# Kernel tuning notes

Measured on AMD Instinct MI355X. Metric: run time of the kernel, lower is better.

Reference implementation:

```python
import jax, jax.numpy as jnp
import numpy as np

B, KPLUS1, D = 64, 513, 1024

def setup_inputs() -> dict:
    key = jax.random.key(0)
    k1, k2, k3 = jax.random.split(key, 3)
    x = jax.random.normal(k1, (B, KPLUS1, D), dtype=jnp.float32)
    # glorot-style scaled init for faithfulness in magnitude
    dense_weights = jax.random.normal(k2, (2 * D, D), dtype=jnp.float32) * (1.0 / np.sqrt(2 * D))
    dot_bias = jax.random.normal(k3, (D, 1), dtype=jnp.float32) * (1.0 / np.sqrt(D))
    return {"x": x, "dense_weights": dense_weights, "dot_bias": dot_bias}

def reference(x, dense_weights, dot_bias):
    # x: [B, K+1, D]; x[:,0] = sentence encoding u, x[:,1:] = knowledge z_t
    u = x[:, 0, :]            # [B, D]
    z = x[:, 1:, :]           # [B, K, D]
    d = z.shape[-1]
    # concat(z_t, u) @ W1 == z @ W1[:D] + u @ W1[D:], broadcast over K
    # (mathematically identical to the tile+concat+matmul in the original)
    w_z = dense_weights[:d, :]   # [D, D]
    w_u = dense_weights[d:, :]   # [D, D]
    m = jnp.tanh(jnp.einsum('bkd,de->bke', z, w_z)
                 + jnp.einsum('bd,de->be', u, w_u)[:, None, :])  # [B, K, D]
    q = jnp.einsum('bke,e->bk', m, dot_bias[:, 0])               # [B, K]
    return jax.nn.softmax(q, axis=-1)                            # [B, K]
```

## Files before the change

kernel.cpp:

```cpp
#include <hip/hip_runtime.h>
#include <hip/hip_bf16.h>


typedef __attribute__((ext_vector_type(8))) short short8;
typedef __attribute__((ext_vector_type(8))) _Float16 half8;
typedef __attribute__((ext_vector_type(4))) float f32x4;
typedef unsigned short ushort_t;

typedef const __attribute__((address_space(1))) void gvoid_t;
typedef __attribute__((address_space(3))) void lvoid_t;

__device__ __forceinline__ ushort_t f2bf(float f) {
    unsigned u = __float_as_uint(f);
    unsigned r = u + 0x7FFFu + ((u >> 16) & 1u);
    return (ushort_t)(r >> 16);
}
__device__ __forceinline__ float bf2f(ushort_t h) {
    return __uint_as_float(((unsigned)h) << 16);
}

__global__ __launch_bounds__(256) void k_prep_z16(const float* __restrict__ x,
                                                  _Float16* __restrict__ z_h) {
    const int idx8 = blockIdx.x * 256 + threadIdx.x;
    const int m = idx8 >> 7;
    const int c = (idx8 & 127) * 8;
    const int b = m >> 9, k = m & 511;
    const float* src = x + ((size_t)(b * 513 + 1 + k) << 10) + c;
    const float4 v0 = *(const float4*)src;
    const float4 v1 = *(const float4*)(src + 4);
    float vv[8] = {v0.x, v0.y, v0.z, v0.w, v1.x, v1.y, v1.z, v1.w};
    half8 hv;
#pragma unroll
    for (int i = 0; i < 8; ++i) hv[i] = (_Float16)vv[i];
    *(half8*)(z_h + (size_t)m * 1024 + c) = hv;
}

__global__ void k_prep_w16(const float* __restrict__ w,
                           _Float16* __restrict__ wzt) {
    __shared__ _Float16 th[64][66];
    const int k0 = blockIdx.x * 64;
    const int n0 = blockIdx.y * 64;
    const int t = threadIdx.x;
    const int lr = t >> 6;
    const int lc = t & 63;
#pragma unroll
    for (int r = 0; r < 16; ++r) {
        int kk = r * 4 + lr;
        th[kk][lc] = (_Float16)w[(size_t)(k0 + kk) * 1024 + n0 + lc];
    }
    __syncthreads();
#pragma unroll
    for (int r = 0; r < 16; ++r) {
        int nn = r * 4 + lr;
        wzt[(size_t)(n0 + nn) * 1024 + k0 + lc] = th[lc][nn];
    }
}

__global__ void k_hu(const float* __restrict__ x,
                     const float* __restrict__ w,
                     float* __restrict__ hu) {
    __shared__ float us[1024];
    const int b = blockIdx.y;
    const int e = blockIdx.x * 256 + threadIdx.x;
    for (int i = threadIdx.x; i < 1024; i += 256)
        us[i] = x[(size_t)b * 513 * 1024 + i];
    __syncthreads();
    const float* wu = w + (size_t)1024 * 1024;
    float acc = 0.f;
#pragma unroll 8
    for (int d = 0; d < 1024; ++d)
        acc = fmaf(us[d], wu[(size_t)d * 1024 + e], acc);
    hu[b * 1024 + e] = acc;
}

__global__ __launch_bounds__(256) void k_gemm6(
        const _Float16* __restrict__ z_h,
        const _Float16* __restrict__ wzt,
        const float* __restrict__ hu,
        const float* __restrict__ bias,
        float* __restrict__ qp) {
    __shared__ __align__(16) _Float16 As[128 * 64];
    __shared__ __align__(16) _Float16 Bs[128 * 64];
    __shared__ float qred[2][2][64];

    const int t = threadIdx.x;
    const int mtile = blockIdx.x;
    const int ntile = blockIdx.y;
    const int wid = t >> 6;
    const int l = t & 63;
    const int wm = wid >> 1;
    const int wn = wid & 1;
    const int lr = l & 15;
    const int g = l >> 4;

    const int rl = l >> 3;
    const int chunk = (l & 7) ^ rl;
    const int half = wid & 1;
    const _Float16* gsrc;
    _Float16* ldsT;
    if (wid < 2) {
        gsrc = z_h + (size_t)(mtile * 128 + half * 64 + rl) * 1024 + chunk * 8;
        ldsT = As + half * 4096;
    } else {
        gsrc = wzt + (size_t)(ntile * 128 + half * 64 + rl) * 1024 + chunk * 8;
        ldsT = Bs + half * 4096;
    }

    f32x4 acc[4][4] = {};

    for (int k0 = 0; k0 < 1024; k0 += 64) {
#pragma unroll
        for (int j = 0; j < 8; ++j) {
            __builtin_amdgcn_global_load_lds(
                (gvoid_t*)(gsrc + k0 + j * 8192),
                (lvoid_t*)((char*)ldsT + j * 1024),
                16, 0, 0);
        }
        __syncthreads();

#pragma unroll
        for (int ks = 0; ks < 2; ++ks) {
            half8 ah[4], bh[4];
            const int so = ((ks * 4 + g) ^ (lr & 7)) * 16;
#pragma unroll
            for (int i = 0; i < 4; ++i) {
                ah[i] = *(const half8*)((const char*)As + (wm * 64 + i * 16 + lr) * 128 + so);
                bh[i] = *(const half8*)((const char*)Bs + (wn * 64 + i * 16 + lr) * 128 + so);
            }
#pragma unroll
            for (int mi = 0; mi < 4; ++mi)
#pragma unroll
                for (int ni = 0; ni < 4; ++ni)
                    acc[mi][ni] = __builtin_amdgcn_mfma_f32_16x16x32_f16(
                        ah[mi], bh[ni], acc[mi][ni], 0, 0, 0);
        }
        __syncthreads();
    }

    const int lg = l >> 4;
    const int bbatch = mtile >> 2;
    float hu4[4], bias4[4];
#pragma unroll
    for (int ni = 0; ni < 4; ++ni) {
        int e = ntile * 128 + wn * 64 + ni * 16 + lr;
        hu4[ni] = hu[bbatch * 1024 + e];
        bias4[ni] = bias[e];
    }
#pragma unroll
    for (int mi = 0; mi < 4; ++mi) {
#pragma unroll
        for (int j = 0; j < 4; ++j) {
            float v = 0.f;
#pragma unroll
            for (int ni = 0; ni < 4; ++ni)
                v += tanhf(acc[mi][ni][j] + hu4[ni]) * bias4[ni];
            v += __shfl_xor(v, 1);
            v += __shfl_xor(v, 2);
            v += __shfl_xor(v, 4);
            v += __shfl_xor(v, 8);
            if (lr == 0)
                qred[wm][wn][mi * 16 + lg * 4 + j] = v;
        }
    }
    __syncthreads();
    if (t < 128) {
        const int wmr = t >> 6;
        const int rr = t & 63;
        float q = qred[wmr][0][rr] + qred[wmr][1][rr];
        qp[(size_t)ntile * 32768 + mtile * 128 + t] = q;
    }
}

__global__ void k_prep_w(const float* __restrict__ w,
                         ushort_t* __restrict__ wzt_hi,
                         ushort_t* __restrict__ wzt_lo) {
    __shared__ ushort_t th[64][66];
    __shared__ ushort_t tl[64][66];
    const int k0 = blockIdx.x * 64;
    const int n0 = blockIdx.y * 64;
    const int t = threadIdx.x;
    const int lr = t >> 6;
    const int lc = t & 63;
#pragma unroll
    for (int r = 0; r < 16; ++r) {
        int kk = r * 4 + lr;
        float f = w[(size_t)(k0 + kk) * 1024 + n0 + lc];
        ushort_t hi = f2bf(f);
        ushort_t lo = f2bf(f - bf2f(hi));
        th[kk][lc] = hi;
        tl[kk][lc] = lo;
    }
    __syncthreads();
#pragma unroll
    for (int r = 0; r < 16; ++r) {
        int nn = r * 4 + lr;
        wzt_hi[(size_t)(n0 + nn) * 1024 + k0 + lc] = th[lc][nn];
        wzt_lo[(size_t)(n0 + nn) * 1024 + k0 + lc] = tl[lc][nn];
    }
}

__global__ __launch_bounds__(256) void k_gemm(
        const float* __restrict__ x,
        const ushort_t* __restrict__ wzt_hi,
        const ushort_t* __restrict__ wzt_lo,
        const float* __restrict__ hu,
        const float* __restrict__ bias,
        float* __restrict__ qp) {
    __shared__ ushort_t As_hi[128][40];
    __shared__ ushort_t As_lo[128][40];
    __shared__ ushort_t Bs_hi[128][40];
    __shared__ ushort_t Bs_lo[128][40];
    __shared__ float qred[2][2][64];

    const int t = threadIdx.x;
    const int mtile = blockIdx.x;
    const int ntile = blockIdx.y;
    const int wid = t >> 6;
    const int l = t & 63;
    const int wm = wid >> 1;
    const int wn = wid & 1;

    f32x4 acc[4][4] = {};

    const int arow = t >> 3;
    const int acol = (t & 7) * 4;
    size_t abase[4];
#pragma unroll
    for (int it = 0; it < 4; ++it) {
        int m = mtile * 128 + arow + it * 32;
        int bb = m >> 9;
        int kk = m & 511;
        abase[it] = ((size_t)(bb * 513 + 1 + kk)) * 1024 + acol;
    }
    const int brow = t >> 2;
    const int bcol = (t & 3) * 8;
    const size_t bbase = (size_t)(ntile * 128 + brow) * 1024 + bcol;

    for (int k0 = 0; k0 < 1024; k0 += 32) {
#pragma unroll
        for (int it = 0; it < 4; ++it) {
            const float4 v = *(const float4*)(x + abase[it] + k0);
            ushort4 hv, lv;
            hv.x = f2bf(v.x); lv.x = f2bf(v.x - bf2f(hv.x));
            hv.y = f2bf(v.y); lv.y = f2bf(v.y - bf2f(hv.y));
            hv.z = f2bf(v.z); lv.z = f2bf(v.z - bf2f(hv.z));
            hv.w = f2bf(v.w); lv.w = f2bf(v.w - bf2f(hv.w));
            const int row = arow + it * 32;
            *(ushort4*)&As_hi[row][acol] = hv;
            *(ushort4*)&As_lo[row][acol] = lv;
        }
#pragma unroll
        for (int it = 0; it < 2; ++it) {
            const int row = brow + it * 64;
            const uint4 vh = *(const uint4*)(wzt_hi + bbase + (size_t)it * 64 * 1024 + k0);
            const uint4 vl = *(const uint4*)(wzt_lo + bbase + (size_t)it * 64 * 1024 + k0);
            *(uint4*)&Bs_hi[row][bcol] = vh;
            *(uint4*)&Bs_lo[row][bcol] = vl;
        }
        __syncthreads();

        const int lr = l & 15;
        const int lk = (l >> 4) * 8;
        short8 ah[4], al[4], bh[4], bl[4];
#pragma unroll
        for (int i = 0; i < 4; ++i) {
            ah[i] = *(const short8*)&As_hi[wm * 64 + i * 16 + lr][lk];
            al[i] = *(const short8*)&As_lo[wm * 64 + i * 16 + lr][lk];
            bh[i] = *(const short8*)&Bs_hi[wn * 64 + i * 16 + lr][lk];
            bl[i] = *(const short8*)&Bs_lo[wn * 64 + i * 16 + lr][lk];
        }
#pragma unroll
        for (int mi = 0; mi < 4; ++mi)
#pragma unroll
            for (int ni = 0; ni < 4; ++ni) {
                acc[mi][ni] = __builtin_amdgcn_mfma_f32_16x16x32_bf16(ah[mi], bh[ni], acc[mi][ni], 0, 0, 0);
                acc[mi][ni] = __builtin_amdgcn_mfma_f32_16x16x32_bf16(ah[mi], bl[ni], acc[mi][ni], 0, 0, 0);
                acc[mi][ni] = __builtin_amdgcn_mfma_f32_16x16x32_bf16(al[mi], bh[ni], acc[mi][ni], 0, 0, 0);
            }
        __syncthreads();
    }

    const int lr = l & 15;
    const int lg = l >> 4;
    const int bbatch = mtile >> 2;
    float hu4[4], bias4[4];
#pragma unroll
    for (int ni = 0; ni < 4; ++ni) {
        int e = ntile * 128 + wn * 64 + ni * 16 + lr;
        hu4[ni] = hu[bbatch * 1024 + e];
        bias4[ni] = bias[e];
    }
#pragma unroll
    for (int mi = 0; mi < 4; ++mi) {
#pragma unroll
        for (int j = 0; j < 4; ++j) {
            float v = 0.f;
#pragma unroll
            for (int ni = 0; ni < 4; ++ni)
                v += tanhf(acc[mi][ni][j] + hu4[ni]) * bias4[ni];
            v += __shfl_xor(v, 1);
            v += __shfl_xor(v, 2);
            v += __shfl_xor(v, 4);
            v += __shfl_xor(v, 8);
            if (lr == 0)
                qred[wm][wn][mi * 16 + lg * 4 + j] = v;
        }
    }
    __syncthreads();
    if (t < 128) {
        const int wmr = t >> 6;
        const int rr = t & 63;
        float q = qred[wmr][0][rr] + qred[wmr][1][rr];
        qp[(size_t)ntile * 32768 + mtile * 128 + t] = q;
    }
}

__global__ void k_softmax(const float* __restrict__ qp, float* __restrict__ out,
                          int nt) {
    const int b = blockIdx.x;
    const int k = threadIdx.x;
    float q = 0.f;
    for (int i = 0; i < nt; ++i)
        q += qp[(size_t)i * 32768 + b * 512 + k];

    __shared__ float redm[8];
    __shared__ float reds[8];
    const int wid = k >> 6;

    float m = q;
#pragma unroll
    for (int off = 32; off >= 1; off >>= 1)
        m = fmaxf(m, __shfl_xor(m, off));
    if ((k & 63) == 0) redm[wid] = m;
    __syncthreads();
    m = redm[0];
#pragma unroll
    for (int i = 1; i < 8; ++i) m = fmaxf(m, redm[i]);

    float p = expf(q - m);
    float s = p;
#pragma unroll
    for (int off = 32; off >= 1; off >>= 1)
        s += __shfl_xor(s, off);
    if ((k & 63) == 0) reds[wid] = s;
    __syncthreads();
    s = 0.f;
#pragma unroll
    for (int i = 0; i < 8; ++i) s += reds[i];

    out[b * 512 + k] = p / s;
}

extern "C" void kernel_launch(void* const* d_in, const int* in_sizes, int n_in,
                              void* d_out, int out_size, void* d_ws, size_t ws_size,
                              hipStream_t stream) {
    const float* x    = (const float*)d_in[0];
    const float* w    = (const float*)d_in[1];
    const float* bias = (const float*)d_in[2];
    float* out = (float*)d_out;

    char* ws = (char*)d_ws;
    const size_t ZN = (size_t)32768 * 1024;

    const size_t need = ZN * sizeof(_Float16)
                      + (size_t)1024 * 1024 * sizeof(_Float16)
                      + (size_t)64 * 1024 * sizeof(float)
                      + (size_t)8 * 32768 * sizeof(float);

    if (ws_size >= need) {
        _Float16* z_h = (_Float16*)ws;
        _Float16* wzt = z_h + ZN;
        float*    hu  = (float*)(wzt + (size_t)1024 * 1024);
        float*    qp  = hu + (size_t)64 * 1024;

        k_prep_z16<<<16384, 256, 0, stream>>>(x, z_h);
        k_prep_w16<<<dim3(16, 16), 256, 0, stream>>>(w, wzt);
        k_hu<<<dim3(4, 64), 256, 0, stream>>>(x, w, hu);
        k_gemm6<<<dim3(256, 8), 256, 0, stream>>>(z_h, wzt, hu, bias, qp);
        k_softmax<<<64, 512, 0, stream>>>(qp, out, 8);
    } else {
        ushort_t* wzt_hi = (ushort_t*)ws;
        ushort_t* wzt_lo = wzt_hi + (size_t)1024 * 1024;
        float* hu = (float*)(ws + (size_t)4 * 1024 * 1024);
        float* qp = hu + (size_t)64 * 1024;

        k_prep_w<<<dim3(16, 16), 256, 0, stream>>>(w, wzt_hi, wzt_lo);
        k_hu<<<dim3(4, 64), 256, 0, stream>>>(x, w, hu);
        k_gemm<<<dim3(256, 8), 256, 0, stream>>>(x, wzt_hi, wzt_lo, hu, bias, qp);
        k_softmax<<<64, 512, 0, stream>>>(qp, out, 8);
    }
}
```

Measured before the change: 204.6 us.

## Enlarge GEMM block tile to 256x256 with 512 threads and fast tanh

The fused GEMM+tanh+dot kernel now uses 256x256 output tiles with 8 waves, each wave computing a 128x64 subtile. This doubles operand reuse per LDS load and halves the number of N-tiles, so there are fewer partial-q slabs for the softmax to sum. The epilogue's tanhf is replaced with an exp-based approximation to cut transcendental cost. In exchange the kernel uses 64 KB of LDS and about 128 accumulator registers per lane, and launches only 512 blocks, which may lower occupancy and tail balance.

```diff
diff --git a/kernel.cpp b/kernel.cpp
--- a/kernel.cpp
+++ b/kernel.cpp
@@ -17,6 +17,10 @@
 }
 __device__ __forceinline__ float bf2f(ushort_t h) {
     return __uint_as_float(((unsigned)h) << 16);
+}
+__device__ __forceinline__ float tanh_fast(float x) {
+    float e = __expf(2.f * x);
+    return 1.f - 2.f / (e + 1.f);
 }
 
 __global__ __launch_bounds__(256) void k_prep_z16(const float* __restrict__ x,
@@ -73,101 +77,102 @@
     hu[b * 1024 + e] = acc;
 }
 
-__global__ __launch_bounds__(256) void k_gemm6(
+__global__ __launch_bounds__(512, 2) void k_gemm9(
         const _Float16* __restrict__ z_h,
         const _Float16* __restrict__ wzt,
         const float* __restrict__ hu,
         const float* __restrict__ bias,
         float* __restrict__ qp) {
-    __shared__ __align__(16) _Float16 As[128 * 64];
-    __shared__ __align__(16) _Float16 Bs[128 * 64];
-    __shared__ float qred[2][2][64];
+    __shared__ __align__(16) _Float16 As[256 * 64];
+    __shared__ __align__(16) _Float16 Bs[256 * 64];
+    __shared__ float qred[2][4][128];
 
     const int t = threadIdx.x;
     const int mtile = blockIdx.x;
     const int ntile = blockIdx.y;
     const int wid = t >> 6;
     const int l = t & 63;
-    const int wm = wid >> 1;
-    const int wn = wid & 1;
+    const int wm = wid >> 2;
+    const int wn = wid & 3;
     const int lr = l & 15;
     const int g = l >> 4;
 
     const int rl = l >> 3;
     const int chunk = (l & 7) ^ rl;
-    const int half = wid & 1;
+    const int w4 = wid & 3;
     const _Float16* gsrc;
     _Float16* ldsT;
-    if (wid < 2) {
-        gsrc = z_h + (size_t)(mtile * 128 + half * 64 + rl) * 1024 + chunk * 8;
-        ldsT = As + half * 4096;
+    if (wid < 4) {
+        gsrc = z_h + (size_t)(mtile * 256 + w4 * 64 + rl) * 1024 + chunk * 8;
+        ldsT = As + w4 * 4096;
     } else {
-        gsrc = wzt + (size_t)(ntile * 128 + half * 64 + rl) * 1024 + chunk * 8;
-        ldsT = Bs + half * 4096;
-    }
-
-    f32x4 acc[4][4] = {};
+        gsrc = wzt + (size_t)(ntile * 256 + w4 * 64 + rl) * 1024 + chunk * 8;
+        ldsT = Bs + w4 * 4096;
+    }
+
+    f32x4 acc[8][4] = {};
 
     for (int k0 = 0; k0 < 1024; k0 += 64) {
 #pragma unroll
         for (int j = 0; j < 8; ++j) {
             __builtin_amdgcn_global_load_lds(
                 (gvoid_t*)(gsrc + k0 + j * 8192),
-                (lvoid_t*)((char*)ldsT + j * 1024),
+                (lvoid_t*)((char*)ldsT + j * 1024 + l * 16),
                 16, 0, 0);
         }
         __syncthreads();
 
 #pragma unroll
         for (int ks = 0; ks < 2; ++ks) {
-            half8 ah[4], bh[4];
+            half8 afr[8], bfr[4];
             const int so = ((ks * 4 + g) ^ (lr & 7)) * 16;
 #pragma unroll
-            for (int i = 0; i < 4; ++i) {
-                ah[i] = *(const half8*)((const char*)As + (wm * 64 + i * 16 + lr) * 128 + so);
-                bh[i] = *(const half8*)((const char*)Bs + (wn * 64 + i * 16 + lr) * 128 + so);
-            }
-#pragma unroll
-            for (int mi = 0; mi < 4; ++mi)
+            for (int ni = 0; ni < 4; ++ni)
+                bfr[ni] = *(const half8*)((const char*)Bs + (wn * 64 + ni * 16 + lr) * 128 + so);
+#pragma unroll
+            for (int mi = 0; mi < 8; ++mi)
+                afr[mi] = *(const half8*)((const char*)As + (wm * 128 + mi * 16 + lr) * 128 + so);
+#pragma unroll
+            for (int mi = 0; mi < 8; ++mi)
 #pragma unroll
                 for (int ni = 0; ni < 4; ++ni)
                     acc[mi][ni] = __builtin_amdgcn_mfma_f32_16x16x32_f16(
-                        ah[mi], bh[ni], acc[mi][ni], 0, 0, 0);
+                        afr[mi], bfr[ni], acc[mi][ni], 0, 0, 0);
         }
         __syncthreads();
     }
 
-    const int lg = l >> 4;
-    const int bbatch = mtile >> 2;
+    const int bb = mtile >> 1;
     float hu4[4], bias4[4];
 #pragma unroll
     for (int ni = 0; ni < 4; ++ni) {
-        int e = ntile * 128 + wn * 64 + ni * 16 + lr;
-        hu4[ni] = hu[bbatch * 1024 + e];
+        int e = ntile * 256 + wn * 64 + ni * 16 + lr;
+        hu4[ni] = hu[bb * 1024 + e];
         bias4[ni] = bias[e];
     }
 #pragma unroll
-    for (int mi = 0; mi < 4; ++mi) {
+    for (int mi = 0; mi < 8; ++mi) {
 #pragma unroll
         for (int j = 0; j < 4; ++j) {
             float v = 0.f;
 #pragma unroll
             for (int ni = 0; ni < 4; ++ni)
-                v += tanhf(acc[mi][ni][j] + hu4[ni]) * bias4[ni];
+                v += tanh_fast(acc[mi][ni][j] + hu4[ni]) * bias4[ni];
             v += __shfl_xor(v, 1);
             v += __shfl_xor(v, 2);
             v += __shfl_xor(v, 4);
             v += __shfl_xor(v, 8);
             if (lr == 0)
-                qred[wm][wn][mi * 16 + lg * 4 + j] = v;
-        }
-    }
-    __syncthreads();
-    if (t < 128) {
-        const int wmr = t >> 6;
-        const int rr = t & 63;
-        float q = qred[wmr][0][rr] + qred[wmr][1][rr];
-        qp[(size_t)ntile * 32768 + mtile * 128 + t] = q;
+                qred[wm][wn][mi * 16 + g * 4 + j] = v;
+        }
+    }
+    __syncthreads();
+    if (t < 256) {
+        const int wmr = t >> 7;
+        const int rr = t & 127;
+        float q = qred[wmr][0][rr] + qred[wmr][1][rr]
+                + qred[wmr][2][rr] + qred[wmr][3][rr];
+        qp[(size_t)ntile * 32768 + mtile * 256 + t] = q;
     }
 }
 
@@ -310,8 +315,8 @@
     if (t < 128) {
         const int wmr = t >> 6;
         const int rr = t & 63;
-        float q = qred[wmr][0][rr] + qred[wmr][1][rr];
-        qp[(size_t)ntile * 32768 + mtile * 128 + t] = q;
+        float qv = qred[wmr][0][rr] + qred[wmr][1][rr];
+        qp[(size_t)ntile * 32768 + mtile * 128 + t] = qv;
     }
 }
 
@@ -365,7 +370,7 @@
     const size_t need = ZN * sizeof(_Float16)
                       + (size_t)1024 * 1024 * sizeof(_Float16)
                       + (size_t)64 * 1024 * sizeof(float)
-                      + (size_t)8 * 32768 * sizeof(float);
+                      + (size_t)4 * 32768 * sizeof(float);
 
     if (ws_size >= need) {
         _Float16* z_h = (_Float16*)ws;
@@ -376,8 +381,8 @@
         k_prep_z16<<<16384, 256, 0, stream>>>(x, z_h);
         k_prep_w16<<<dim3(16, 16), 256, 0, stream>>>(w, wzt);
         k_hu<<<dim3(4, 64), 256, 0, stream>>>(x, w, hu);
-        k_gemm6<<<dim3(256, 8), 256, 0, stream>>>(z_h, wzt, hu, bias, qp);
-        k_softmax<<<64, 512, 0, stream>>>(qp, out, 8);
+        k_gemm9<<<dim3(128, 4), 512, 0, stream>>>(z_h, wzt, hu, bias, qp);
+        k_softmax<<<64, 512, 0, stream>>>(qp, out, 4);
     } else {
         ushort_t* wzt_hi = (ushort_t*)ws;
         ushort_t* wzt_lo = wzt_hi + (size_t)1024 * 1024;
```

New measurement: 180.6 us. -11.8%, faster.
